# Kernel tuning notes

Hardware: AMD Instinct MI355X
Metric: run time of the kernel (lower is better)

Reference implementation:

```python
import jax, jax.numpy as jnp
import jax.lax as lax
import numpy as np

G = 128    # number of asset groups (batch)
A = 100    # n_assets per group
WIN = 10   # window_size
FD = 16    # feature_dim
H = 128    # hidden_dim


def setup_inputs() -> dict:
    key = jax.random.key(0)
    ks = jax.random.split(key, 12)
    N = G * A
    def glorot(k, shape, fan_in):
        return (jax.random.normal(k, shape, jnp.float32) / np.sqrt(fan_in)).astype(jnp.float32)
    return {
        "x": jax.random.normal(ks[0], (N, WIN, FD), jnp.float32),
        "W1": glorot(ks[1], (WIN * FD, H), WIN * FD),
        "b1": jnp.zeros((H,), jnp.float32),
        "W2": glorot(ks[2], (H, H), H),
        "b2": jnp.zeros((H,), jnp.float32),
        "W3": glorot(ks[3], (H, H), H),
        "b3": jnp.zeros((H,), jnp.float32),
        "cw1": glorot(ks[4], (H, 1, 1, 3), 3),      # conv2d_1 weight [out,in,kh,kw]
        "cb1": jnp.zeros((H,), jnp.float32),
        "cw2": glorot(ks[5], (1, H, 1, 3), 3 * H),  # conv2d_2 weight
        "cb2": jnp.zeros((1,), jnp.float32),
    }


def _corrcoef(r):
    xc = r - r.mean(axis=1, keepdims=True)
    cov = xc @ xc.T                      # divisor cancels in correlation
    d = jnp.sqrt(jnp.diag(cov))
    return cov / (d[:, None] * d[None, :])


def _conv1x3(h, w, b):
    # h: [1,C,N,H]; kernel (1,3), padding (0,1) -> NCHW conv
    out = lax.conv_general_dilated(h, w, (1, 1), ((0, 0), (1, 1)),
                                   dimension_numbers=("NCHW", "OIHW", "NCHW"))
    return out + b[None, :, None, None]


def reference(x, W1, b1, W2, b2, W3, b3, cw1, cb1, cw2, cb2):
    # block-diagonal adjacency == independent per-group adjacencies
    returns = x[:, :, -1].reshape(G, A, WIN)
    corr = jax.vmap(_corrcoef)(returns)                  # [G,A,A]
    adj = 1.0 - jnp.abs(corr) + jnp.eye(A, dtype=x.dtype)
    dinv = 1.0 / jnp.sqrt(adj.sum(axis=-1))              # [G,A]
    norm_adj = dinv[:, :, None] * adj * dinv[:, None, :] # D^-1/2 A D^-1/2

    feats = x.reshape(G, A, WIN * FD)
    h = jax.nn.relu(jnp.einsum("gij,gjf->gif", norm_adj, feats) @ W1 + b1)
    h = jax.nn.relu(jnp.einsum("gij,gjh->gih", norm_adj, h) @ W2 + b2)
    h = jax.nn.relu(jnp.einsum("gij,gjh->gih", norm_adj, h) @ W3 + b3)

    h = h.reshape(1, 1, G * A, H)                        # [1,1,N,H]
    h = jax.nn.relu(_conv1x3(h, cw1, cb1))               # [1,H,N,H]
    out = _conv1x3(h, cw2, cb2)                          # [1,1,N,H]
    return out[0, 0]                                     # [N,H]
```

## Files before the change

### kernel.cpp

```cpp
#include <hip/hip_runtime.h>

#define G   128
#define A   100
#define WIN 10
#define FD  16
#define H   128
#define NROWS (G*A)
#define K1  (WIN*FD)

typedef __attribute__((ext_vector_type(8))) short short8;
typedef __attribute__((ext_vector_type(4))) short short4v;
typedef __attribute__((ext_vector_type(4))) float floatx4;

struct BfPair { short h, l; };

__device__ inline unsigned short f2bf(float f) {
    unsigned u = __float_as_uint(f);
    u += 0x7fff + ((u >> 16) & 1);
    return (unsigned short)(u >> 16);
}
__device__ inline float bf2f(unsigned short h) {
    return __uint_as_float(((unsigned)h) << 16);
}
__device__ inline BfPair split1(float v) {
    BfPair p;
    unsigned short hb = f2bf(v);
    p.h = (short)hb;
    p.l = (short)f2bf(v - bf2f(hb));
    return p;
}

__global__ __launch_bounds__(256) void k_nadj(const float* __restrict__ x,
                                              float* __restrict__ nadj) {
    __shared__ float xcT[WIN][104];
    __shared__ float invn[A];
    __shared__ float adjs[A][101];
    __shared__ float dinv[A];
    const int g = blockIdx.x;
    const int t = threadIdx.x;

    for (int idx = t; idx < A * WIN; idx += 256) {
        int a = idx / WIN, w = idx % WIN;
        xcT[w][a] = x[((g * A + a) * WIN + w) * FD + (FD - 1)];
    }
    __syncthreads();
    if (t < A) {
        float m = 0.f;
        #pragma unroll
        for (int w = 0; w < WIN; w++) m += xcT[w][t];
        m *= (1.0f / WIN);
        float ss = 0.f;
        #pragma unroll
        for (int w = 0; w < WIN; w++) {
            float v = xcT[w][t] - m;
            xcT[w][t] = v;
            ss += v * v;
        }
        invn[t] = rsqrtf(ss);
    }
    __syncthreads();
    for (int tt2 = t; tt2 < 2500; tt2 += 256) {
        int ti = tt2 / 50, tj = tt2 % 50;
        int i0 = 2 * ti, j0v = 2 * tj;
        float d00 = 0.f, d01 = 0.f, d10 = 0.f, d11 = 0.f;
        #pragma unroll
        for (int w = 0; w < WIN; w++) {
            float2 xi = *(const float2*)&xcT[w][i0];
            float2 xj = *(const float2*)&xcT[w][j0v];
            d00 = fmaf(xi.x, xj.x, d00); d01 = fmaf(xi.x, xj.y, d01);
            d10 = fmaf(xi.y, xj.x, d10); d11 = fmaf(xi.y, xj.y, d11);
        }
        float ii0 = invn[i0], ii1 = invn[i0 + 1];
        float ij0 = invn[j0v], ij1 = invn[j0v + 1];
        float e = (ti == tj) ? 1.f : 0.f;
        adjs[i0][j0v]         = 1.f - fabsf(d00 * ii0 * ij0) + e;
        adjs[i0][j0v + 1]     = 1.f - fabsf(d01 * ii0 * ij1);
        adjs[i0 + 1][j0v]     = 1.f - fabsf(d10 * ii1 * ij0);
        adjs[i0 + 1][j0v + 1] = 1.f - fabsf(d11 * ii1 * ij1) + e;
    }
    __syncthreads();
    if (t < A) {
        float s = 0.f;
        for (int j = 0; j < A; j++) s += adjs[t][j];
        dinv[t] = rsqrtf(s);
    }
    __syncthreads();
    for (int idx = t; idx < A * A; idx += 256) {
        int i = idx / A, j = idx % A;
        nadj[g * A * A + idx] = dinv[i] * adjs[i][j] * dinv[j];
    }
}

__global__ __launch_bounds__(256) void k_layer(const float* __restrict__ nadj,
                                               const float* __restrict__ X,
                                               const float* __restrict__ W,
                                               const float* __restrict__ bias,
                                               float* __restrict__ Z, int K) {
    __shared__ short Xh[112 * 40], Xl[112 * 40];
    __shared__ short Wh[64 * 40],  Wl[64 * 40];
    __shared__ short Yh[64 * 136], Yl[64 * 136];

    const int g = blockIdx.x;
    const int cbase = blockIdx.y * 64;
    const int t = threadIdx.x;
    const int w = t >> 6, lane = t & 63;
    const int quad = lane >> 4, r16 = lane & 15;

    for (int e = t; e < 480; e += 256) { Xh[4000 + e] = 0; Xl[4000 + e] = 0; }
    for (int e = t; e < 1024; e += 256) {
        int n = e >> 4, k = 112 + (e & 15);
        Yh[n * 136 + k] = 0; Yl[n * 136 + k] = 0;
    }

    floatx4 acc[7];
    #pragma unroll
    for (int i = 0; i < 7; i++) acc[i] = (floatx4)0.f;

    const float* Xg = X + (size_t)g * A * K;
    const int nch = K >> 5;
    for (int c = 0; c < nch; c++) {
        const int k0 = c << 5;
        for (int e = t; e < 400; e += 256) {
            int r = e >> 2, q = e & 3;
            const float* gp = Xg + (size_t)r * K + k0 + q * 8;
            float4 f0 = *(const float4*)gp;
            float4 f1 = *(const float4*)(gp + 4);
            float v[8] = {f0.x, f0.y, f0.z, f0.w, f1.x, f1.y, f1.z, f1.w};
            short8 hh, ll;
            #pragma unroll
            for (int i = 0; i < 8; i++) {
                BfPair p = split1(v[i]);
                hh[i] = p.h; ll[i] = p.l;
            }
            *(short8*)&Xh[r * 40 + q * 8] = hh;
            *(short8*)&Xl[r * 40 + q * 8] = ll;
        }
        for (int e = t; e < 512; e += 256) {
            int kk = e >> 4, n4 = (e & 15) * 4;
            float4 f = *(const float4*)(W + (size_t)(k0 + kk) * H + cbase + n4);
            float v[4] = {f.x, f.y, f.z, f.w};
            #pragma unroll
            for (int i = 0; i < 4; i++) {
                BfPair p = split1(v[i]);
                Wh[(n4 + i) * 40 + kk] = p.h;
                Wl[(n4 + i) * 40 + kk] = p.l;
            }
        }
        __syncthreads();
        short8 bh = *(const short8*)&Wh[(w * 16 + r16) * 40 + quad * 8];
        short8 bl = *(const short8*)&Wl[(w * 16 + r16) * 40 + quad * 8];
        #pragma unroll
        for (int tm = 0; tm < 7; tm++) {
            short8 ah = *(const short8*)&Xh[(tm * 16 + r16) * 40 + quad * 8];
            short8 al = *(const short8*)&Xl[(tm * 16 + r16) * 40 + quad * 8];
            acc[tm] = __builtin_amdgcn_mfma_f32_16x16x32_bf16(ah, bh, acc[tm], 0, 0, 0);
            acc[tm] = __builtin_amdgcn_mfma_f32_16x16x32_bf16(ah, bl, acc[tm], 0, 0, 0);
            acc[tm] = __builtin_amdgcn_mfma_f32_16x16x32_bf16(al, bh, acc[tm], 0, 0, 0);
        }
        __syncthreads();
    }

    const int n = w * 16 + r16;
    #pragma unroll
    for (int tm = 0; tm < 7; tm++) {
        short4v yh, yl;
        #pragma unroll
        for (int rr = 0; rr < 4; rr++) {
            BfPair p = split1(acc[tm][rr]);
            yh[rr] = p.h; yl[rr] = p.l;
        }
        *(short4v*)&Yh[n * 136 + tm * 16 + quad * 4] = yh;
        *(short4v*)&Yl[n * 136 + tm * 16 + quad * 4] = yl;
        acc[tm] = (floatx4)0.f;
    }
    __syncthreads();

    const float* ng = nadj + (size_t)g * A * A;
    for (int c = 0; c < 4; c++) {
        const int k0 = c << 5;
        for (int e = t; e < 400; e += 256) {
            int r = e >> 2, q = e & 3;
            short8 hh, ll;
            #pragma unroll
            for (int i = 0; i < 8; i++) {
                int k = k0 + q * 8 + i;
                float v = (k < A) ? ng[r * A + k] : 0.f;
                BfPair p = split1(v);
                hh[i] = p.h; ll[i] = p.l;
            }
            *(short8*)&Xh[r * 40 + q * 8] = hh;
            *(short8*)&Xl[r * 40 + q * 8] = ll;
        }
        __syncthreads();
        short8 bh = *(const short8*)&Yh[n * 136 + k0 + quad * 8];
        short8 bl = *(const short8*)&Yl[n * 136 + k0 + quad * 8];
        #pragma unroll
        for (int tm = 0; tm < 7; tm++) {
            short8 ah = *(const short8*)&Xh[(tm * 16 + r16) * 40 + quad * 8];
            short8 al = *(const short8*)&Xl[(tm * 16 + r16) * 40 + quad * 8];
            acc[tm] = __builtin_amdgcn_mfma_f32_16x16x32_bf16(ah, bh, acc[tm], 0, 0, 0);
            acc[tm] = __builtin_amdgcn_mfma_f32_16x16x32_bf16(ah, bl, acc[tm], 0, 0, 0);
            acc[tm] = __builtin_amdgcn_mfma_f32_16x16x32_bf16(al, bh, acc[tm], 0, 0, 0);
        }
        __syncthreads();
    }

    const float bv = bias[cbase + n];
    #pragma unroll
    for (int tm = 0; tm < 7; tm++) {
        #pragma unroll
        for (int rr = 0; rr < 4; rr++) {
            int r = tm * 16 + quad * 4 + rr;
            if (r < A)
                Z[((size_t)g * A + r) * H + cbase + n] =
                    fmaxf(0.f, acc[tm][rr] + bv);
        }
    }
}

__global__ __launch_bounds__(256) void k_conv(const float* __restrict__ h3,
                                              const float* __restrict__ cw1,
                                              const float* __restrict__ cb1,
                                              const float* __restrict__ cw2,
                                              const float* __restrict__ cb2,
                                              float* __restrict__ out) {
    __shared__ float wbuf[H][8];
    const int t = threadIdx.x;
    if (t < H) {
        *(float4*)&wbuf[t][0] = make_float4(cw1[3 * t], cw1[3 * t + 1], cw1[3 * t + 2], cb1[t]);
        *(float4*)&wbuf[t][4] = make_float4(cw2[3 * t], cw2[3 * t + 1], cw2[3 * t + 2], 0.f);
    }
    __syncthreads();

    const int wave = t >> 6, lane = t & 63;
    const int n = blockIdx.x * 8 + wave * 2 + (lane >> 5);
    const int q = lane & 31;
    const int j0 = q * 4;
    const float* hr = h3 + (size_t)n * H;

    float hh[8];
    if (q == 0) {
        float4 a  = *(const float4*)(hr);
        float2 b2 = *(const float2*)(hr + 4);
        hh[0] = 0.f;  hh[1] = 0.f;  hh[2] = a.x;  hh[3] = a.y;
        hh[4] = a.z;  hh[5] = a.w;  hh[6] = b2.x; hh[7] = b2.y;
    } else if (q == 31) {
        float2 b2 = *(const float2*)(hr + 122);
        float4 a  = *(const float4*)(hr + 124);
        hh[0] = b2.x; hh[1] = b2.y; hh[2] = a.x;  hh[3] = a.y;
        hh[4] = a.z;  hh[5] = a.w;  hh[6] = 0.f;  hh[7] = 0.f;
    } else {
        float4 a  = *(const float4*)(hr + j0 - 2);
        float4 b4 = *(const float4*)(hr + j0 + 2);
        hh[0] = a.x;  hh[1] = a.y;  hh[2] = a.z;  hh[3] = a.w;
        hh[4] = b4.x; hh[5] = b4.y; hh[6] = b4.z; hh[7] = b4.w;
    }
    const float mlo = (q == 0)  ? 0.f : 1.f;
    const float mhi = (q == 31) ? 0.f : 1.f;

    float acc[4] = {0.f, 0.f, 0.f, 0.f};
    #pragma unroll 4
    for (int c = 0; c < H; c++) {
        float4 wA = *(const float4*)&wbuf[c][0];
        float4 wB = *(const float4*)&wbuf[c][4];
        float tt[6];
        #pragma unroll
        for (int m = 0; m < 6; m++)
            tt[m] = fmaxf(0.f, fmaf(wA.z, hh[m + 2],
                               fmaf(wA.y, hh[m + 1],
                               fmaf(wA.x, hh[m], wA.w))));
        tt[0] *= mlo;
        tt[5] *= mhi;
        #pragma unroll
        for (int p = 0; p < 4; p++)
            acc[p] = fmaf(wB.x, tt[p],
                     fmaf(wB.y, tt[p + 1],
                     fmaf(wB.z, tt[p + 2], acc[p])));
    }
    const float c2b = cb2[0];
    *(float4*)(out + (size_t)n * H + j0) =
        make_float4(acc[0] + c2b, acc[1] + c2b, acc[2] + c2b, acc[3] + c2b);
}

extern "C" void kernel_launch(void* const* d_in, const int* in_sizes, int n_in,
                              void* d_out, int out_size, void* d_ws, size_t ws_size,
                              hipStream_t stream) {
    const float* x   = (const float*)d_in[0];
    const float* W1  = (const float*)d_in[1];
    const float* b1  = (const float*)d_in[2];
    const float* W2  = (const float*)d_in[3];
    const float* b2  = (const float*)d_in[4];
    const float* W3  = (const float*)d_in[5];
    const float* b3  = (const float*)d_in[6];
    const float* cw1 = (const float*)d_in[7];
    const float* cb1 = (const float*)d_in[8];
    const float* cw2 = (const float*)d_in[9];
    const float* cb2 = (const float*)d_in[10];
    float* out = (float*)d_out;

    float* ws   = (float*)d_ws;
    float* nadj = ws;
    float* bufA = nadj + (size_t)G * A * A;
    float* bufB = bufA + (size_t)NROWS * H;

    k_nadj<<<G, 256, 0, stream>>>(x, nadj);

    k_layer<<<dim3(G, 2), 256, 0, stream>>>(nadj, x,    W1, b1, bufA, K1);
    k_layer<<<dim3(G, 2), 256, 0, stream>>>(nadj, bufA, W2, b2, bufB, H);
    k_layer<<<dim3(G, 2), 256, 0, stream>>>(nadj, bufB, W3, b3, bufA, H);

    k_conv<<<NROWS / 8, 256, 0, stream>>>(bufA, cw1, cb1, cw2, cb2, out);
}
```

Baseline: 197.0 us.

## Presplit weights and adjacency to bf16 hi/lo once, shrink layer column tiles

```diff
diff --git a/kernel.cpp b/kernel.cpp
--- a/kernel.cpp
+++ b/kernel.cpp
@@ -30,8 +30,48 @@
     return p;
 }
 
+__global__ __launch_bounds__(256) void k_prep(const float* __restrict__ W1,
+                                              const float* __restrict__ W2,
+                                              const float* __restrict__ W3,
+                                              const float* __restrict__ cw1,
+                                              const float* __restrict__ cb1,
+                                              const float* __restrict__ cw2,
+                                              const float* __restrict__ cb2,
+                                              short* __restrict__ Wh,
+                                              short* __restrict__ Wl,
+                                              float* __restrict__ wpack) {
+    const int b = blockIdx.x, t = threadIdx.x;
+    if (b < 26) {
+        int l, kc, K;
+        const float* Wsrc;
+        if (b < 10)      { l = 0; kc = b;      K = K1; Wsrc = W1; }
+        else if (b < 18) { l = 1; kc = b - 10; K = H;  Wsrc = W2; }
+        else             { l = 2; kc = b - 18; K = H;  Wsrc = W3; }
+        short* dh = Wh + l * 128 * 160;
+        short* dl = Wl + l * 128 * 160;
+        for (int e = t; e < 16 * 128; e += 256) {
+            int k = kc * 16 + (e >> 7), n = e & 127;
+            BfPair p = split1(Wsrc[(size_t)k * H + n]);
+            dh[n * 160 + k] = p.h;
+            dl[n * 160 + k] = p.l;
+        }
+        (void)K;
+    } else {
+        for (int e = t; e < 1024; e += 256) {
+            int c = e >> 3, s = e & 7;
+            float v;
+            if (s < 3)       v = cw1[3 * c + s];
+            else if (s == 3) v = cb1[c];
+            else if (s < 7)  v = cw2[3 * c + (s - 4)];
+            else             v = cb2[0];
+            wpack[e] = v;
+        }
+    }
+}
+
 __global__ __launch_bounds__(256) void k_nadj(const float* __restrict__ x,
-                                              float* __restrict__ nadj) {
+                                              short* __restrict__ Sh,
+                                              short* __restrict__ Sl) {
     __shared__ float xcT[WIN][104];
     __shared__ float invn[A];
     __shared__ float adjs[A][101];
@@ -85,41 +125,54 @@
         dinv[t] = rsqrtf(s);
     }
     __syncthreads();
-    for (int idx = t; idx < A * A; idx += 256) {
-        int i = idx / A, j = idx % A;
-        nadj[g * A * A + idx] = dinv[i] * adjs[i][j] * dinv[j];
-    }
-}
-
-__global__ __launch_bounds__(256) void k_layer(const float* __restrict__ nadj,
+    short* sh = Sh + (size_t)g * 112 * 128;
+    short* sl = Sl + (size_t)g * 112 * 128;
+    for (int idx = t; idx < 112 * 128; idx += 256) {
+        int i = idx >> 7, k = idx & 127;
+        float v = (i < A && k < A) ? dinv[i] * adjs[i][k] * dinv[k] : 0.f;
+        BfPair p = split1(v);
+        sh[idx] = p.h;
+        sl[idx] = p.l;
+    }
+}
+
+__global__ __launch_bounds__(256) void k_layer(const short* __restrict__ Sh,
+                                               const short* __restrict__ Sl,
+                                               const short* __restrict__ Whg,
+                                               const short* __restrict__ Wlg,
                                                const float* __restrict__ X,
-                                               const float* __restrict__ W,
                                                const float* __restrict__ bias,
                                                float* __restrict__ Z, int K) {
     __shared__ short Xh[112 * 40], Xl[112 * 40];
-    __shared__ short Wh[64 * 40],  Wl[64 * 40];
-    __shared__ short Yh[64 * 136], Yl[64 * 136];
-
+    __shared__ short Yh[32 * 136], Yl[32 * 136];
     const int g = blockIdx.x;
-    const int cbase = blockIdx.y * 64;
+    const int cbase = blockIdx.y * 32;
     const int t = threadIdx.x;
     const int w = t >> 6, lane = t & 63;
     const int quad = lane >> 4, r16 = lane & 15;
-
-    for (int e = t; e < 480; e += 256) { Xh[4000 + e] = 0; Xl[4000 + e] = 0; }
-    for (int e = t; e < 1024; e += 256) {
+    const int nm = (w < 3) ? 2 : 1;
+    const int m0 = 2 * w;
+
+    for (int e = t; e < 384; e += 256) {
+        int r = 100 + e / 32, c = e % 32;
+        Xh[r * 40 + c] = 0; Xl[r * 40 + c] = 0;
+    }
+    for (int e = t; e < 512; e += 256) {
         int n = e >> 4, k = 112 + (e & 15);
         Yh[n * 136 + k] = 0; Yl[n * 136 + k] = 0;
     }
 
-    floatx4 acc[7];
+    floatx4 acc[2][2];
     #pragma unroll
-    for (int i = 0; i < 7; i++) acc[i] = (floatx4)0.f;
+    for (int i = 0; i < 2; i++)
+        #pragma unroll
+        for (int j = 0; j < 2; j++) acc[i][j] = (floatx4)0.f;
 
     const float* Xg = X + (size_t)g * A * K;
     const int nch = K >> 5;
     for (int c = 0; c < nch; c++) {
         const int k0 = c << 5;
+        __syncthreads();
         for (int e = t; e < 400; e += 256) {
             int r = e >> 2, q = e & 3;
             const float* gp = Xg + (size_t)r * K + k0 + q * 8;
@@ -135,103 +188,89 @@
             *(short8*)&Xh[r * 40 + q * 8] = hh;
             *(short8*)&Xl[r * 40 + q * 8] = ll;
         }
-        for (int e = t; e < 512; e += 256) {
-            int kk = e >> 4, n4 = (e & 15) * 4;
-            float4 f = *(const float4*)(W + (size_t)(k0 + kk) * H + cbase + n4);
-            float v[4] = {f.x, f.y, f.z, f.w};
-            #pragma unroll
-            for (int i = 0; i < 4; i++) {
-                BfPair p = split1(v[i]);
-                Wh[(n4 + i) * 40 + kk] = p.h;
-                Wl[(n4 + i) * 40 + kk] = p.l;
-            }
-        }
         __syncthreads();
-        short8 bh = *(const short8*)&Wh[(w * 16 + r16) * 40 + quad * 8];
-        short8 bl = *(const short8*)&Wl[(w * 16 + r16) * 40 + quad * 8];
-        #pragma unroll
-        for (int tm = 0; tm < 7; tm++) {
-            short8 ah = *(const short8*)&Xh[(tm * 16 + r16) * 40 + quad * 8];
-            short8 al = *(const short8*)&Xl[(tm * 16 + r16) * 40 + quad * 8];
-            acc[tm] = __builtin_amdgcn_mfma_f32_16x16x32_bf16(ah, bh, acc[tm], 0, 0, 0);
-            acc[tm] = __builtin_amdgcn_mfma_f32_16x16x32_bf16(ah, bl, acc[tm], 0, 0, 0);
-            acc[tm] = __builtin_amdgcn_mfma_f32_16x16x32_bf16(al, bh, acc[tm], 0, 0, 0);
-        }
-        __syncthreads();
-    }
-
-    const int n = w * 16 + r16;
+        short8 bh[2], bl[2];
+        #pragma unroll
+        for (int nt = 0; nt < 2; nt++) {
+            size_t wo = (size_t)(cbase + nt * 16 + r16) * 160 + k0 + quad * 8;
+            bh[nt] = *(const short8*)(Whg + wo);
+            bl[nt] = *(const short8*)(Wlg + wo);
+        }
+        for (int mt = 0; mt < nm; mt++) {
+            int xo = ((m0 + mt) * 16 + r16) * 40 + quad * 8;
+            short8 ah = *(const short8*)&Xh[xo];
+            short8 al = *(const short8*)&Xl[xo];
+            #pragma unroll
+            for (int nt = 0; nt < 2; nt++) {
+                acc[mt][nt] = __builtin_amdgcn_mfma_f32_16x16x32_bf16(ah, bh[nt], acc[mt][nt], 0, 0, 0);
+                acc[mt][nt] = __builtin_amdgcn_mfma_f32_16x16x32_bf16(ah, bl[nt], acc[mt][nt], 0, 0, 0);
+                acc[mt][nt] = __builtin_amdgcn_mfma_f32_16x16x32_bf16(al, bh[nt], acc[mt][nt], 0, 0, 0);
+            }
+        }
+    }
+    __syncthreads();
+
+    for (int mt = 0; mt < nm; mt++) {
+        #pragma unroll
+        for (int nt = 0; nt < 2; nt++) {
+            short4v yh4, yl4;
+            #pragma unroll
+            for (int rr = 0; rr < 4; rr++) {
+                BfPair p = split1(acc[mt][nt][rr]);
+                yh4[rr] = p.h; yl4[rr] = p.l;
+            }
+            int off = (nt * 16 + r16) * 136 + (m0 + mt) * 16 + quad * 4;
+            *(short4v*)&Yh[off] = yh4;
+            *(short4v*)&Yl[off] = yl4;
+            acc[mt][nt] = (floatx4)0.f;
+        }
+    }
+    __syncthreads();
+
+    const short* Sgh = Sh + (size_t)g * 112 * 128;
+    const short* Sgl = Sl + (size_t)g * 112 * 128;
     #pragma unroll
-    for (int tm = 0; tm < 7; tm++) {
-        short4v yh, yl;
-        #pragma unroll
-        for (int rr = 0; rr < 4; rr++) {
-            BfPair p = split1(acc[tm][rr]);
-            yh[rr] = p.h; yl[rr] = p.l;
-        }
-        *(short4v*)&Yh[n * 136 + tm * 16 + quad * 4] = yh;
-        *(short4v*)&Yl[n * 136 + tm * 16 + quad * 4] = yl;
-        acc[tm] = (floatx4)0.f;
-    }
-    __syncthreads();
-
-    const float* ng = nadj + (size_t)g * A * A;
     for (int c = 0; c < 4; c++) {
         const int k0 = c << 5;
-        for (int e = t; e < 400; e += 256) {
-            int r = e >> 2, q = e & 3;
-            short8 hh, ll;
-            #pragma unroll
-            for (int i = 0; i < 8; i++) {
-                int k = k0 + q * 8 + i;
-                float v = (k < A) ? ng[r * A + k] : 0.f;
-                BfPair p = split1(v);
-                hh[i] = p.h; ll[i] = p.l;
-            }
-            *(short8*)&Xh[r * 40 + q * 8] = hh;
-            *(short8*)&Xl[r * 40 + q * 8] = ll;
-        }
-        __syncthreads();
-        short8 bh = *(const short8*)&Yh[n * 136 + k0 + quad * 8];
-        short8 bl = *(const short8*)&Yl[n * 136 + k0 + quad * 8];
-        #pragma unroll
-        for (int tm = 0; tm < 7; tm++) {
-            short8 ah = *(const short8*)&Xh[(tm * 16 + r16) * 40 + quad * 8];
-            short8 al = *(const short8*)&Xl[(tm * 16 + r16) * 40 + quad * 8];
-            acc[tm] = __builtin_amdgcn_mfma_f32_16x16x32_bf16(ah, bh, acc[tm], 0, 0, 0);
-            acc[tm] = __builtin_amdgcn_mfma_f32_16x16x32_bf16(ah, bl, acc[tm], 0, 0, 0);
-            acc[tm] = __builtin_amdgcn_mfma_f32_16x16x32_bf16(al, bh, acc[tm], 0, 0, 0);
-        }
-        __syncthreads();
-    }
-
-    const float bv = bias[cbase + n];
+        short8 bh[2], bl[2];
+        #pragma unroll
+        for (int nt = 0; nt < 2; nt++) {
+            int yo = (nt * 16 + r16) * 136 + k0 + quad * 8;
+            bh[nt] = *(const short8*)&Yh[yo];
+            bl[nt] = *(const short8*)&Yl[yo];
+        }
+        for (int mt = 0; mt < nm; mt++) {
+            size_t so = (size_t)((m0 + mt) * 16 + r16) * 128 + k0 + quad * 8;
+            short8 ah = *(const short8*)(Sgh + so);
+            short8 al = *(const short8*)(Sgl + so);
+            #pragma unroll
+            for (int nt = 0; nt < 2; nt++) {
+                acc[mt][nt] = __builtin_amdgcn_mfma_f32_16x16x32_bf16(ah, bh[nt], acc[mt][nt], 0, 0, 0);
+                acc[mt][nt] = __builtin_amdgcn_mfma_f32_16x16x32_bf16(ah, bl[nt], acc[mt][nt], 0, 0, 0);
+                acc[mt][nt] = __builtin_amdgcn_mfma_f32_16x16x32_bf16(al, bh[nt], acc[mt][nt], 0, 0, 0);
+            }
+        }
+    }
+
     #pragma unroll
-    for (int tm = 0; tm < 7; tm++) {
-        #pragma unroll
-        for (int rr = 0; rr < 4; rr++) {
-            int r = tm * 16 + quad * 4 + rr;
-            if (r < A)
-                Z[((size_t)g * A + r) * H + cbase + n] =
-                    fmaxf(0.f, acc[tm][rr] + bv);
+    for (int nt = 0; nt < 2; nt++) {
+        float bv = bias[cbase + nt * 16 + r16];
+        for (int mt = 0; mt < nm; mt++) {
+            #pragma unroll
+            for (int rr = 0; rr < 4; rr++) {
+                int i = (m0 + mt) * 16 + quad * 4 + rr;
+                if (i < A)
+                    Z[((size_t)g * A + i) * H + cbase + nt * 16 + r16] =
+                        fmaxf(0.f, acc[mt][nt][rr] + bv);
+            }
         }
     }
 }
 
 __global__ __launch_bounds__(256) void k_conv(const float* __restrict__ h3,
-                                              const float* __restrict__ cw1,
-                                              const float* __restrict__ cb1,
-                                              const float* __restrict__ cw2,
-                                              const float* __restrict__ cb2,
+                                              const float* __restrict__ wpack,
                                               float* __restrict__ out) {
-    __shared__ float wbuf[H][8];
     const int t = threadIdx.x;
-    if (t < H) {
-        *(float4*)&wbuf[t][0] = make_float4(cw1[3 * t], cw1[3 * t + 1], cw1[3 * t + 2], cb1[t]);
-        *(float4*)&wbuf[t][4] = make_float4(cw2[3 * t], cw2[3 * t + 1], cw2[3 * t + 2], 0.f);
-    }
-    __syncthreads();
-
     const int wave = t >> 6, lane = t & 63;
     const int n = blockIdx.x * 8 + wave * 2 + (lane >> 5);
     const int q = lane & 31;
@@ -259,25 +298,26 @@
     const float mhi = (q == 31) ? 0.f : 1.f;
 
     float acc[4] = {0.f, 0.f, 0.f, 0.f};
-    #pragma unroll 4
+    #pragma unroll 8
     for (int c = 0; c < H; c++) {
-        float4 wA = *(const float4*)&wbuf[c][0];
-        float4 wB = *(const float4*)&wbuf[c][4];
+        const float* wp = wpack + c * 8;
+        float w0 = wp[0], w1 = wp[1], w2 = wp[2], b = wp[3];
+        float v0 = wp[4], v1 = wp[5], v2 = wp[6];
         float tt[6];
         #pragma unroll
         for (int m = 0; m < 6; m++)
-            tt[m] = fmaxf(0.f, fmaf(wA.z, hh[m + 2],
-                               fmaf(wA.y, hh[m + 1],
-                               fmaf(wA.x, hh[m], wA.w))));
+            tt[m] = fmaxf(0.f, fmaf(w2, hh[m + 2],
+                               fmaf(w1, hh[m + 1],
+                               fmaf(w0, hh[m], b))));
         tt[0] *= mlo;
         tt[5] *= mhi;
         #pragma unroll
         for (int p = 0; p < 4; p++)
-            acc[p] = fmaf(wB.x, tt[p],
-                     fmaf(wB.y, tt[p + 1],
-                     fmaf(wB.z, tt[p + 2], acc[p])));
-    }
-    const float c2b = cb2[0];
+            acc[p] = fmaf(v0, tt[p],
+                     fmaf(v1, tt[p + 1],
+                     fmaf(v2, tt[p + 2], acc[p])));
+    }
+    const float c2b = wpack[7];
     *(float4*)(out + (size_t)n * H + j0) =
         make_float4(acc[0] + c2b, acc[1] + c2b, acc[2] + c2b, acc[3] + c2b);
 }
@@ -298,16 +338,20 @@
     const float* cb2 = (const float*)d_in[10];
     float* out = (float*)d_out;
 
-    float* ws   = (float*)d_ws;
-    float* nadj = ws;
-    float* bufA = nadj + (size_t)G * A * A;
-    float* bufB = bufA + (size_t)NROWS * H;
-
-    k_nadj<<<G, 256, 0, stream>>>(x, nadj);
-
-    k_layer<<<dim3(G, 2), 256, 0, stream>>>(nadj, x,    W1, b1, bufA, K1);
-    k_layer<<<dim3(G, 2), 256, 0, stream>>>(nadj, bufA, W2, b2, bufB, H);
-    k_layer<<<dim3(G, 2), 256, 0, stream>>>(nadj, bufB, W3, b3, bufA, H);
-
-    k_conv<<<NROWS / 8, 256, 0, stream>>>(bufA, cw1, cb1, cw2, cb2, out);
-}
+    short* Sh = (short*)d_ws;
+    short* Sl = Sh + (size_t)G * 112 * 128;
+    short* Wh = Sl + (size_t)G * 112 * 128;
+    short* Wl = Wh + 3 * 128 * 160;
+    float* wpack = (float*)(Wl + 3 * 128 * 160);
+    float* bufA  = wpack + 1024;
+    float* bufB  = bufA + (size_t)NROWS * H;
+
+    k_prep<<<27, 256, 0, stream>>>(W1, W2, W3, cw1, cb1, cw2, cb2, Wh, Wl, wpack);
+    k_nadj<<<G, 256, 0, stream>>>(x, Sh, Sl);
+
+    k_layer<<<dim3(G, 4), 256, 0, stream>>>(Sh, Sl, Wh,             Wl,             x,    b1, bufA, K1);
+    k_layer<<<dim3(G, 4), 256, 0, stream>>>(Sh, Sl, Wh + 128 * 160, Wl + 128 * 160, bufA, b2, bufB, H);
+    k_layer<<<dim3(G, 4), 256, 0, stream>>>(Sh, Sl, Wh + 256 * 160, Wl + 256 * 160, bufB, b3, bufA, H);
+
+    k_conv<<<NROWS / 8, 256, 0, stream>>>(bufA, wpack, out);
+}
```

Result: no change. 200.6 us (+1.8%).

## Fuse adjacency, three GCN layers and conv into one per-group megakernel

Applied to the files above, without the earlier changes.

```diff
diff --git a/kernel.cpp b/kernel.cpp
--- a/kernel.cpp
+++ b/kernel.cpp
@@ -8,6 +8,11 @@
 #define NROWS (G*A)
 #define K1  (WIN*FD)
 
+#define SST 136
+#define YST 136
+#define AST 40
+#define H3ST 132
+
 typedef __attribute__((ext_vector_type(8))) short short8;
 typedef __attribute__((ext_vector_type(4))) short short4v;
 typedef __attribute__((ext_vector_type(4))) float floatx4;
@@ -30,256 +35,269 @@
     return p;
 }
 
-__global__ __launch_bounds__(256) void k_nadj(const float* __restrict__ x,
-                                              float* __restrict__ nadj) {
+__global__ __launch_bounds__(1024) void k_mega(
+    const float* __restrict__ x,
+    const float* __restrict__ W1, const float* __restrict__ b1,
+    const float* __restrict__ W2, const float* __restrict__ b2,
+    const float* __restrict__ W3, const float* __restrict__ b3,
+    const float* __restrict__ cw1, const float* __restrict__ cb1,
+    const float* __restrict__ cw2, const float* __restrict__ cb2,
+    float* __restrict__ out)
+{
+    __shared__ short Ybuf[2 * 128 * YST];
+    __shared__ short Sbuf[2 * 112 * SST];
+    __shared__ short Abuf[2 * 112 * AST];
+    __shared__ float wbuf[H][8];
     __shared__ float xcT[WIN][104];
     __shared__ float invn[A];
-    __shared__ float adjs[A][101];
     __shared__ float dinv[A];
-    const int g = blockIdx.x;
+
+    short* Yh = Ybuf;            short* Yl = Ybuf + 128 * YST;
+    short* Sh = Sbuf;            short* Sl = Sbuf + 112 * SST;
+    short* Ah = Abuf;            short* Al = Abuf + 112 * AST;
+    float* adjs = (float*)Ybuf;
+    float* h3f  = (float*)Sbuf;
+
+    const int g = blockIdx.x >> 1, half = blockIdx.x & 1;
     const int t = threadIdx.x;
-
-    for (int idx = t; idx < A * WIN; idx += 256) {
-        int a = idx / WIN, w = idx % WIN;
-        xcT[w][a] = x[((g * A + a) * WIN + w) * FD + (FD - 1)];
+    const int wvid = t >> 6, lane = t & 63;
+    const int quad = lane >> 4, r16 = lane & 15;
+
+    if (t < H) {
+        *(float4*)&wbuf[t][0] = make_float4(cw1[3*t], cw1[3*t+1], cw1[3*t+2], cb1[t]);
+        *(float4*)&wbuf[t][4] = make_float4(cw2[3*t], cw2[3*t+1], cw2[3*t+2], cb2[0]);
+    }
+    for (int e = t; e < A * WIN; e += 1024) {
+        int a = e / WIN, wv = e % WIN;
+        xcT[wv][a] = x[((g * A + a) * WIN + wv) * FD + (FD - 1)];
     }
     __syncthreads();
     if (t < A) {
         float m = 0.f;
         #pragma unroll
-        for (int w = 0; w < WIN; w++) m += xcT[w][t];
+        for (int wv = 0; wv < WIN; wv++) m += xcT[wv][t];
         m *= (1.0f / WIN);
         float ss = 0.f;
         #pragma unroll
-        for (int w = 0; w < WIN; w++) {
-            float v = xcT[w][t] - m;
-            xcT[w][t] = v;
+        for (int wv = 0; wv < WIN; wv++) {
+            float v = xcT[wv][t] - m;
+            xcT[wv][t] = v;
             ss += v * v;
         }
         invn[t] = rsqrtf(ss);
     }
     __syncthreads();
-    for (int tt2 = t; tt2 < 2500; tt2 += 256) {
-        int ti = tt2 / 50, tj = tt2 % 50;
+    for (int e = t; e < 2500; e += 1024) {
+        int ti = e / 50, tj = e % 50;
         int i0 = 2 * ti, j0v = 2 * tj;
         float d00 = 0.f, d01 = 0.f, d10 = 0.f, d11 = 0.f;
         #pragma unroll
-        for (int w = 0; w < WIN; w++) {
-            float2 xi = *(const float2*)&xcT[w][i0];
-            float2 xj = *(const float2*)&xcT[w][j0v];
+        for (int wv = 0; wv < WIN; wv++) {
+            float2 xi = *(const float2*)&xcT[wv][i0];
+            float2 xj = *(const float2*)&xcT[wv][j0v];
             d00 = fmaf(xi.x, xj.x, d00); d01 = fmaf(xi.x, xj.y, d01);
             d10 = fmaf(xi.y, xj.x, d10); d11 = fmaf(xi.y, xj.y, d11);
         }
         float ii0 = invn[i0], ii1 = invn[i0 + 1];
         float ij0 = invn[j0v], ij1 = invn[j0v + 1];
-        float e = (ti == tj) ? 1.f : 0.f;
-        adjs[i0][j0v]         = 1.f - fabsf(d00 * ii0 * ij0) + e;
-        adjs[i0][j0v + 1]     = 1.f - fabsf(d01 * ii0 * ij1);
-        adjs[i0 + 1][j0v]     = 1.f - fabsf(d10 * ii1 * ij0);
-        adjs[i0 + 1][j0v + 1] = 1.f - fabsf(d11 * ii1 * ij1) + e;
+        float e2 = (ti == tj) ? 1.f : 0.f;
+        adjs[i0 * 101 + j0v]           = 1.f - fabsf(d00 * ii0 * ij0) + e2;
+        adjs[i0 * 101 + j0v + 1]       = 1.f - fabsf(d01 * ii0 * ij1);
+        adjs[(i0 + 1) * 101 + j0v]     = 1.f - fabsf(d10 * ii1 * ij0);
+        adjs[(i0 + 1) * 101 + j0v + 1] = 1.f - fabsf(d11 * ii1 * ij1) + e2;
     }
     __syncthreads();
     if (t < A) {
         float s = 0.f;
-        for (int j = 0; j < A; j++) s += adjs[t][j];
+        for (int j = 0; j < A; j++) s += adjs[t * 101 + j];
         dinv[t] = rsqrtf(s);
     }
     __syncthreads();
-    for (int idx = t; idx < A * A; idx += 256) {
-        int i = idx / A, j = idx % A;
-        nadj[g * A * A + idx] = dinv[i] * adjs[i][j] * dinv[j];
-    }
-}
-
-__global__ __launch_bounds__(256) void k_layer(const float* __restrict__ nadj,
-                                               const float* __restrict__ X,
-                                               const float* __restrict__ W,
-                                               const float* __restrict__ bias,
-                                               float* __restrict__ Z, int K) {
-    __shared__ short Xh[112 * 40], Xl[112 * 40];
-    __shared__ short Wh[64 * 40],  Wl[64 * 40];
-    __shared__ short Yh[64 * 136], Yl[64 * 136];
-
-    const int g = blockIdx.x;
-    const int cbase = blockIdx.y * 64;
-    const int t = threadIdx.x;
-    const int w = t >> 6, lane = t & 63;
-    const int quad = lane >> 4, r16 = lane & 15;
-
-    for (int e = t; e < 480; e += 256) { Xh[4000 + e] = 0; Xl[4000 + e] = 0; }
-    for (int e = t; e < 1024; e += 256) {
+    for (int e = t; e < 112 * 64; e += 1024) {
+        int m = e >> 6, k2 = (e & 63) * 2;
+        float v0 = (m < A && k2 < A)     ? dinv[m] * adjs[m * 101 + k2]     * dinv[k2]     : 0.f;
+        float v1 = (m < A && k2 + 1 < A) ? dinv[m] * adjs[m * 101 + k2 + 1] * dinv[k2 + 1] : 0.f;
+        BfPair p0 = split1(v0), p1 = split1(v1);
+        *(short2*)&Sh[m * SST + k2] = make_short2(p0.h, p1.h);
+        *(short2*)&Sl[m * SST + k2] = make_short2(p0.l, p1.l);
+    }
+    if (t < 384) {
+        int r = 100 + (t >> 5), c = t & 31;
+        Ah[r * AST + c] = 0; Al[r * AST + c] = 0;
+    }
+    __syncthreads();
+    for (int e = t; e < 2048; e += 1024) {
         int n = e >> 4, k = 112 + (e & 15);
-        Yh[n * 136 + k] = 0; Yl[n * 136 + k] = 0;
-    }
-
-    floatx4 acc[7];
-    #pragma unroll
-    for (int i = 0; i < 7; i++) acc[i] = (floatx4)0.f;
-
-    const float* Xg = X + (size_t)g * A * K;
-    const int nch = K >> 5;
-    for (int c = 0; c < nch; c++) {
-        const int k0 = c << 5;
-        for (int e = t; e < 400; e += 256) {
-            int r = e >> 2, q = e & 3;
-            const float* gp = Xg + (size_t)r * K + k0 + q * 8;
-            float4 f0 = *(const float4*)gp;
-            float4 f1 = *(const float4*)(gp + 4);
-            float v[8] = {f0.x, f0.y, f0.z, f0.w, f1.x, f1.y, f1.z, f1.w};
-            short8 hh, ll;
+        Yh[n * YST + k] = 0; Yl[n * YST + k] = 0;
+    }
+
+    const int ntA  = wvid & 7;
+    const int mtlo = (wvid < 8) ? 0 : 4;
+    const int mcnt = (wvid < 8) ? 4 : 3;
+    const int mtB  = wvid >> 1;
+    const int ntB0 = (wvid & 1) * 4;
+
+    for (int layer = 0; layer < 3; layer++) {
+        const float* Wg = (layer == 0) ? W1 : (layer == 1) ? W2 : W3;
+        const float* bg = (layer == 0) ? b1 : (layer == 1) ? b2 : b3;
+        const int nch = (layer == 0) ? 5 : 4;
+
+        floatx4 acc[4];
+        #pragma unroll
+        for (int i = 0; i < 4; i++) acc[i] = (floatx4)0.f;
+
+        for (int c = 0; c < nch; c++) {
+            const int k0 = c << 5;
+            short8 bh, bl;
+            {
+                const float* wp = Wg + (size_t)(k0 + quad * 8) * H + ntA * 16 + r16;
+                #pragma unroll
+                for (int i = 0; i < 8; i++) {
+                    BfPair p = split1(wp[(size_t)i * H]);
+                    bh[i] = p.h; bl[i] = p.l;
+                }
+            }
+            if (layer == 0) {
+                __syncthreads();
+                if (t < 800) {
+                    int r = t >> 3, q = t & 7;
+                    float4 f = *(const float4*)(x + (size_t)(g * A + r) * K1 + k0 + q * 4);
+                    float v[4] = {f.x, f.y, f.z, f.w};
+                    short4v hh, ll;
+                    #pragma unroll
+                    for (int i = 0; i < 4; i++) {
+                        BfPair p = split1(v[i]);
+                        hh[i] = p.h; ll[i] = p.l;
+                    }
+                    *(short4v*)&Ah[r * AST + q * 4] = hh;
+                    *(short4v*)&Al[r * AST + q * 4] = ll;
+                }
+                __syncthreads();
+                for (int mi = 0; mi < mcnt; mi++) {
+                    int mt = mtlo + mi;
+                    short8 ah = *(const short8*)&Ah[(mt * 16 + r16) * AST + quad * 8];
+                    short8 al = *(const short8*)&Al[(mt * 16 + r16) * AST + quad * 8];
+                    acc[mi] = __builtin_amdgcn_mfma_f32_16x16x32_bf16(ah, bh, acc[mi], 0, 0, 0);
+                    acc[mi] = __builtin_amdgcn_mfma_f32_16x16x32_bf16(ah, bl, acc[mi], 0, 0, 0);
+                    acc[mi] = __builtin_amdgcn_mfma_f32_16x16x32_bf16(al, bh, acc[mi], 0, 0, 0);
+                }
+            } else {
+                for (int mi = 0; mi < mcnt; mi++) {
+                    int mt = mtlo + mi;
+                    short8 ah = *(const short8*)&Yh[(mt * 16 + r16) * YST + k0 + quad * 8];
+                    short8 al = *(const short8*)&Yl[(mt * 16 + r16) * YST + k0 + quad * 8];
+                    acc[mi] = __builtin_amdgcn_mfma_f32_16x16x32_bf16(ah, bh, acc[mi], 0, 0, 0);
+                    acc[mi] = __builtin_amdgcn_mfma_f32_16x16x32_bf16(ah, bl, acc[mi], 0, 0, 0);
+                    acc[mi] = __builtin_amdgcn_mfma_f32_16x16x32_bf16(al, bh, acc[mi], 0, 0, 0);
+                }
+            }
+        }
+        __syncthreads();
+
+        for (int mi = 0; mi < mcnt; mi++) {
+            int mt = mtlo + mi;
+            short4v yh4, yl4;
             #pragma unroll
-            for (int i = 0; i < 8; i++) {
-                BfPair p = split1(v[i]);
-                hh[i] = p.h; ll[i] = p.l;
-            }
-            *(short8*)&Xh[r * 40 + q * 8] = hh;
-            *(short8*)&Xl[r * 40 + q * 8] = ll;
-        }
-        for (int e = t; e < 512; e += 256) {
-            int kk = e >> 4, n4 = (e & 15) * 4;
-            float4 f = *(const float4*)(W + (size_t)(k0 + kk) * H + cbase + n4);
-            float v[4] = {f.x, f.y, f.z, f.w};
+            for (int rr = 0; rr < 4; rr++) {
+                BfPair p = split1(acc[mi][rr]);
+                yh4[rr] = p.h; yl4[rr] = p.l;
+            }
+            int off = (ntA * 16 + r16) * YST + mt * 16 + quad * 4;
+            *(short4v*)&Yh[off] = yh4;
+            *(short4v*)&Yl[off] = yl4;
+        }
+        __syncthreads();
+
+        floatx4 accB[4];
+        #pragma unroll
+        for (int i = 0; i < 4; i++) accB[i] = (floatx4)0.f;
+        if (mtB < 7) {
             #pragma unroll
-            for (int i = 0; i < 4; i++) {
-                BfPair p = split1(v[i]);
-                Wh[(n4 + i) * 40 + kk] = p.h;
-                Wl[(n4 + i) * 40 + kk] = p.l;
+            for (int c = 0; c < 4; c++) {
+                const int k0 = c << 5;
+                short8 ah = *(const short8*)&Sh[(mtB * 16 + r16) * SST + k0 + quad * 8];
+                short8 al = *(const short8*)&Sl[(mtB * 16 + r16) * SST + k0 + quad * 8];
+                #pragma unroll
+                for (int j = 0; j < 4; j++) {
+                    int nt = ntB0 + j;
+                    short8 yh8 = *(const short8*)&Yh[(nt * 16 + r16) * YST + k0 + quad * 8];
+                    short8 yl8 = *(const short8*)&Yl[(nt * 16 + r16) * YST + k0 + quad * 8];
+                    accB[j] = __builtin_amdgcn_mfma_f32_16x16x32_bf16(ah, yh8, accB[j], 0, 0, 0);
+                    accB[j] = __builtin_amdgcn_mfma_f32_16x16x32_bf16(ah, yl8, accB[j], 0, 0, 0);
+                    accB[j] = __builtin_amdgcn_mfma_f32_16x16x32_bf16(al, yh8, accB[j], 0, 0, 0);
+                }
             }
         }
         __syncthreads();
-        short8 bh = *(const short8*)&Wh[(w * 16 + r16) * 40 + quad * 8];
-        short8 bl = *(const short8*)&Wl[(w * 16 + r16) * 40 + quad * 8];
-        #pragma unroll
-        for (int tm = 0; tm < 7; tm++) {
-            short8 ah = *(const short8*)&Xh[(tm * 16 + r16) * 40 + quad * 8];
-            short8 al = *(const short8*)&Xl[(tm * 16 + r16) * 40 + quad * 8];
-            acc[tm] = __builtin_amdgcn_mfma_f32_16x16x32_bf16(ah, bh, acc[tm], 0, 0, 0);
-            acc[tm] = __builtin_amdgcn_mfma_f32_16x16x32_bf16(ah, bl, acc[tm], 0, 0, 0);
-            acc[tm] = __builtin_amdgcn_mfma_f32_16x16x32_bf16(al, bh, acc[tm], 0, 0, 0);
+
+        if (mtB < 7) {
+            #pragma unroll
+            for (int j = 0; j < 4; j++) {
+                int n = (ntB0 + j) * 16 + r16;
+                float bv = bg[n];
+                #pragma unroll
+                for (int rr = 0; rr < 4; rr++) {
+                    int m = mtB * 16 + quad * 4 + rr;
+                    float v = fmaxf(0.f, accB[j][rr] + bv);
+                    if (layer < 2) {
+                        BfPair p = split1(v);
+                        Yh[m * YST + n] = p.h;
+                        Yl[m * YST + n] = p.l;
+                    } else if (m < A) {
+                        h3f[m * H3ST + n] = v;
+                    }
+                }
+            }
         }
         __syncthreads();
     }
 
-    const int n = w * 16 + r16;
-    #pragma unroll
-    for (int tm = 0; tm < 7; tm++) {
-        short4v yh, yl;
-        #pragma unroll
-        for (int rr = 0; rr < 4; rr++) {
-            BfPair p = split1(acc[tm][rr]);
-            yh[rr] = p.h; yl[rr] = p.l;
-        }
-        *(short4v*)&Yh[n * 136 + tm * 16 + quad * 4] = yh;
-        *(short4v*)&Yl[n * 136 + tm * 16 + quad * 4] = yl;
-        acc[tm] = (floatx4)0.f;
-    }
-    __syncthreads();
-
-    const float* ng = nadj + (size_t)g * A * A;
-    for (int c = 0; c < 4; c++) {
-        const int k0 = c << 5;
-        for (int e = t; e < 400; e += 256) {
-            int r = e >> 2, q = e & 3;
-            short8 hh, ll;
-            #pragma unroll
-            for (int i = 0; i < 8; i++) {
-                int k = k0 + q * 8 + i;
-                float v = (k < A) ? ng[r * A + k] : 0.f;
-                BfPair p = split1(v);
-                hh[i] = p.h; ll[i] = p.l;
-            }
-            *(short8*)&Xh[r * 40 + q * 8] = hh;
-            *(short8*)&Xl[r * 40 + q * 8] = ll;
-        }
-        __syncthreads();
-        short8 bh = *(const short8*)&Yh[n * 136 + k0 + quad * 8];
-        short8 bl = *(const short8*)&Yl[n * 136 + k0 + quad * 8];
-        #pragma unroll
-        for (int tm = 0; tm < 7; tm++) {
-            short8 ah = *(const short8*)&Xh[(tm * 16 + r16) * 40 + quad * 8];
-            short8 al = *(const short8*)&Xl[(tm * 16 + r16) * 40 + quad * 8];
-            acc[tm] = __builtin_amdgcn_mfma_f32_16x16x32_bf16(ah, bh, acc[tm], 0, 0, 0);
-            acc[tm] = __builtin_amdgcn_mfma_f32_16x16x32_bf16(ah, bl, acc[tm], 0, 0, 0);
-            acc[tm] = __builtin_amdgcn_mfma_f32_16x16x32_bf16(al, bh, acc[tm], 0, 0, 0);
-        }
-        __syncthreads();
-    }
-
-    const float bv = bias[cbase + n];
-    #pragma unroll
-    for (int tm = 0; tm < 7; tm++) {
-        #pragma unroll
-        for (int rr = 0; rr < 4; rr++) {
-            int r = tm * 16 + quad * 4 + rr;
-            if (r < A)
-                Z[((size_t)g * A + r) * H + cbase + n] =
-                    fmaxf(0.f, acc[tm][rr] + bv);
-        }
-    }
-}
-
-__global__ __launch_bounds__(256) void k_conv(const float* __restrict__ h3,
-                                              const float* __restrict__ cw1,
-                                              const float* __restrict__ cb1,
-                                              const float* __restrict__ cw2,
-                                              const float* __restrict__ cb2,
-                                              float* __restrict__ out) {
-    __shared__ float wbuf[H][8];
-    const int t = threadIdx.x;
-    if (t < H) {
-        *(float4*)&wbuf[t][0] = make_float4(cw1[3 * t], cw1[3 * t + 1], cw1[3 * t + 2], cb1[t]);
-        *(float4*)&wbuf[t][4] = make_float4(cw2[3 * t], cw2[3 * t + 1], cw2[3 * t + 2], 0.f);
-    }
-    __syncthreads();
-
-    const int wave = t >> 6, lane = t & 63;
-    const int n = blockIdx.x * 8 + wave * 2 + (lane >> 5);
-    const int q = lane & 31;
+    const int slot = t >> 5, q = t & 31;
     const int j0 = q * 4;
-    const float* hr = h3 + (size_t)n * H;
-
-    float hh[8];
-    if (q == 0) {
-        float4 a  = *(const float4*)(hr);
-        float2 b2 = *(const float2*)(hr + 4);
-        hh[0] = 0.f;  hh[1] = 0.f;  hh[2] = a.x;  hh[3] = a.y;
-        hh[4] = a.z;  hh[5] = a.w;  hh[6] = b2.x; hh[7] = b2.y;
-    } else if (q == 31) {
-        float2 b2 = *(const float2*)(hr + 122);
-        float4 a  = *(const float4*)(hr + 124);
-        hh[0] = b2.x; hh[1] = b2.y; hh[2] = a.x;  hh[3] = a.y;
-        hh[4] = a.z;  hh[5] = a.w;  hh[6] = 0.f;  hh[7] = 0.f;
-    } else {
-        float4 a  = *(const float4*)(hr + j0 - 2);
-        float4 b4 = *(const float4*)(hr + j0 + 2);
-        hh[0] = a.x;  hh[1] = a.y;  hh[2] = a.z;  hh[3] = a.w;
-        hh[4] = b4.x; hh[5] = b4.y; hh[6] = b4.z; hh[7] = b4.w;
-    }
     const float mlo = (q == 0)  ? 0.f : 1.f;
     const float mhi = (q == 31) ? 0.f : 1.f;
-
-    float acc[4] = {0.f, 0.f, 0.f, 0.f};
-    #pragma unroll 4
-    for (int c = 0; c < H; c++) {
-        float4 wA = *(const float4*)&wbuf[c][0];
-        float4 wB = *(const float4*)&wbuf[c][4];
-        float tt[6];
-        #pragma unroll
-        for (int m = 0; m < 6; m++)
-            tt[m] = fmaxf(0.f, fmaf(wA.z, hh[m + 2],
-                               fmaf(wA.y, hh[m + 1],
-                               fmaf(wA.x, hh[m], wA.w))));
-        tt[0] *= mlo;
-        tt[5] *= mhi;
-        #pragma unroll
-        for (int p = 0; p < 4; p++)
-            acc[p] = fmaf(wB.x, tt[p],
-                     fmaf(wB.y, tt[p + 1],
-                     fmaf(wB.z, tt[p + 2], acc[p])));
-    }
-    const float c2b = cb2[0];
-    *(float4*)(out + (size_t)n * H + j0) =
-        make_float4(acc[0] + c2b, acc[1] + c2b, acc[2] + c2b, acc[3] + c2b);
+    const float c2b = wbuf[0][7];
+    #pragma unroll
+    for (int it = 0; it < 2; it++) {
+        int rl = it * 32 + slot;
+        if (rl < 50) {
+            int r = half * 50 + rl;
+            const float* hr = h3f + (size_t)r * H3ST;
+            float hh[8];
+            if (q == 0) {
+                hh[0] = 0.f; hh[1] = 0.f;
+                #pragma unroll
+                for (int i = 0; i < 6; i++) hh[2 + i] = hr[i];
+            } else if (q == 31) {
+                #pragma unroll
+                for (int i = 0; i < 6; i++) hh[i] = hr[122 + i];
+                hh[6] = 0.f; hh[7] = 0.f;
+            } else {
+                #pragma unroll
+                for (int i = 0; i < 8; i++) hh[i] = hr[j0 - 2 + i];
+            }
+            float acc4[4] = {0.f, 0.f, 0.f, 0.f};
+            #pragma unroll 4
+            for (int c = 0; c < H; c++) {
+                float4 wA = *(const float4*)&wbuf[c][0];
+                float4 wB = *(const float4*)&wbuf[c][4];
+                float tt[6];
+                #pragma unroll
+                for (int m2 = 0; m2 < 6; m2++)
+                    tt[m2] = fmaxf(0.f, fmaf(wA.z, hh[m2 + 2],
+                                        fmaf(wA.y, hh[m2 + 1],
+                                        fmaf(wA.x, hh[m2], wA.w))));
+                tt[0] *= mlo; tt[5] *= mhi;
+                #pragma unroll
+                for (int p2 = 0; p2 < 4; p2++)
+                    acc4[p2] = fmaf(wB.x, tt[p2],
+                               fmaf(wB.y, tt[p2 + 1],
+                               fmaf(wB.z, tt[p2 + 2], acc4[p2])));
+            }
+            *(float4*)(out + ((size_t)g * A + r) * H + j0) =
+                make_float4(acc4[0] + c2b, acc4[1] + c2b, acc4[2] + c2b, acc4[3] + c2b);
+        }
+    }
 }
 
 extern "C" void kernel_launch(void* const* d_in, const int* in_sizes, int n_in,
@@ -298,16 +316,6 @@
     const float* cb2 = (const float*)d_in[10];
     float* out = (float*)d_out;
 
-    float* ws   = (float*)d_ws;
-    float* nadj = ws;
-    float* bufA = nadj + (size_t)G * A * A;
-    float* bufB = bufA + (size_t)NROWS * H;
-
-    k_nadj<<<G, 256, 0, stream>>>(x, nadj);
-
-    k_layer<<<dim3(G, 2), 256, 0, stream>>>(nadj, x,    W1, b1, bufA, K1);
-    k_layer<<<dim3(G, 2), 256, 0, stream>>>(nadj, bufA, W2, b2, bufB, H);
-    k_layer<<<dim3(G, 2), 256, 0, stream>>>(nadj, bufB, W3, b3, bufA, H);
-
-    k_conv<<<NROWS / 8, 256, 0, stream>>>(bufA, cw1, cb1, cw2, cb2, out);
-}
+    k_mega<<<G * 2, 1024, 0, stream>>>(x, W1, b1, W2, b2, W3, b3,
+                                       cw1, cb1, cw2, cb2, out);
+}
```

New measurement: 166.8 us. -15.4%, faster.
